# Kernel tuning notes

Measured on AMD Instinct MI355X. Metric: run time of the kernel, lower is better.

## Reference

```python
import jax, jax.numpy as jnp
import numpy as np

B_SZ, T_LEN, VOCAB, R = 32, 500, 8192, 4

def setup_inputs() -> dict:
    key = jax.random.key(0)
    k1, k2, k3 = jax.random.split(key, 3)
    x = jax.random.normal(k1, (B_SZ, T_LEN, VOCAB), dtype=jnp.float32)
    Y = jax.random.randint(k2, (B_SZ, T_LEN), 0, VOCAB, dtype=jnp.int64)
    B_buf = jax.random.normal(k3, (R + 1,), dtype=jnp.float32)
    return {"x": x, "Y": Y, "B_buf": B_buf}

def reference(x, Y, B_buf):
    # Supervised InfoNCE at batch_num == 0 (A_neg buffer reset to -inf, B <- B_).
    x = jnp.clip(x, -30.0, 30.0)
    Bsz, T, V = x.shape
    # cross[i, j] = sum_t x[j, t, Y[i, t]]  (score of sample j's logits under sample i's targets)
    g = jnp.take_along_axis(x[None, :, :, :], Y[:, None, :, None], axis=3)[..., 0]  # [B_i, B_j, T]
    cross = g.sum(axis=2)  # [B, B]
    numerator = jnp.diagonal(cross)  # [B], cross[i,i] == gather(x_i, Y_i).sum
    # logaddexp(numerator[i], logsumexp_{j!=i} cross[i,j]) == logsumexp_j cross[i,j]
    denominator = jax.scipy.special.logsumexp(cross, axis=1)  # [B]
    # A_neg[i] = -inf at batch_num 0, so only B_buf[0] contributes extra mass
    denominator_ = jnp.logaddexp(denominator, B_buf[0])
    loss_terms = numerator - denominator_  # [B]
    correct = jnp.exp(loss_terms).sum() * T
    loss = -loss_terms.sum()
    loss = loss / (Bsz * T)  # avg=True; l2_reg=0
    return loss, correct
```

## Files before the change

kernel.cpp:

```cpp
#include <hip/hip_runtime.h>
#include <math.h>

#define B_SZ  32
#define T_LEN 500
#define VOCAB 8192

__global__ __launch_bounds__(256)
void infonce_cross_kernel(const float* __restrict__ x,
                          const int*   __restrict__ Y,
                          float*       __restrict__ cross) {
    const int j = blockIdx.x;
    const int i = blockIdx.y;
    const float* __restrict__ xj = x + (size_t)j * T_LEN * VOCAB;
    const int*   __restrict__ Yi = Y + i * T_LEN;

    float acc = 0.0f;
    for (int t = threadIdx.x; t < T_LEN; t += 256) {
        const int y = Yi[t];
        float v = xj[(size_t)t * VOCAB + y];
        v = fminf(fmaxf(v, -30.0f), 30.0f);
        acc += v;
    }

    #pragma unroll
    for (int off = 32; off > 0; off >>= 1)
        acc += __shfl_down(acc, off, 64);

    __shared__ float ws[4];
    const int lane = threadIdx.x & 63;
    const int wid  = threadIdx.x >> 6;
    if (lane == 0) ws[wid] = acc;
    __syncthreads();
    if (threadIdx.x == 0) {
        cross[i * B_SZ + j] = ws[0] + ws[1] + ws[2] + ws[3];
    }
}

__global__ __launch_bounds__(64)
void infonce_finalize_kernel(const float* __restrict__ cross,
                             const float* __restrict__ B_buf,
                             float*       __restrict__ out) {
    __shared__ double lt[B_SZ];
    const int i = threadIdx.x;

    if (i < B_SZ) {
        double m = -INFINITY;
        #pragma unroll
        for (int jj = 0; jj < B_SZ; ++jj) {
            double c = (double)cross[i * B_SZ + jj];
            m = fmax(m, c);
        }
        double s = 0.0;
        #pragma unroll
        for (int jj = 0; jj < B_SZ; ++jj) {
            s += exp((double)cross[i * B_SZ + jj] - m);
        }
        const double lse = m + log(s);
        const double b0 = (double)B_buf[0];
        const double hi = fmax(lse, b0);
        const double lo = fmin(lse, b0);
        const double den = hi + log1p(exp(lo - hi));
        const double num = (double)cross[i * B_SZ + i];
        lt[i] = num - den;
    }
    __syncthreads();

    if (i == 0) {
        double sum_lt = 0.0, sum_exp = 0.0;
        #pragma unroll
        for (int k = 0; k < B_SZ; ++k) {
            sum_lt  += lt[k];
            sum_exp += exp(lt[k]);
        }
        out[0] = (float)(-sum_lt / ((double)B_SZ * (double)T_LEN));
        out[1] = (float)(sum_exp * (double)T_LEN);
    }
}

extern "C" void kernel_launch(void* const* d_in, const int* in_sizes, int n_in,
                              void* d_out, int out_size, void* d_ws, size_t ws_size,
                              hipStream_t stream) {
    const float* x     = (const float*)d_in[0];
    const int*   Y     = (const int*)  d_in[1];
    const float* B_buf = (const float*)d_in[2];
    float* out = (float*)d_out;
    float* cross = (float*)d_ws;

    dim3 grid(B_SZ, B_SZ);
    infonce_cross_kernel<<<grid, 256, 0, stream>>>(x, Y, cross);
    infonce_finalize_kernel<<<1, 64, 0, stream>>>(cross, B_buf, out);
}
```

Baseline: 21.02 us.

## Fuse cross and finalize kernels with last-block atomic counter

```diff
diff --git a/kernel.cpp b/kernel.cpp
--- a/kernel.cpp
+++ b/kernel.cpp
@@ -1,79 +1,87 @@
 #include <hip/hip_runtime.h>
 #include <math.h>
 
-#define B_SZ  32
-#define T_LEN 500
-#define VOCAB 8192
+#define B_SZ   32
+#define T_LEN  500
+#define VOCAB  8192
+#define NBLK   (B_SZ * B_SZ)
 
-__global__ __launch_bounds__(256)
-void infonce_cross_kernel(const float* __restrict__ x,
+__global__ __launch_bounds__(512)
+void infonce_fused_kernel(const float* __restrict__ x,
                           const int*   __restrict__ Y,
-                          float*       __restrict__ cross) {
-    const int j = blockIdx.x;
-    const int i = blockIdx.y;
-    const float* __restrict__ xj = x + (size_t)j * T_LEN * VOCAB;
-    const int*   __restrict__ Yi = Y + i * T_LEN;
+                          const float* __restrict__ B_buf,
+                          float*       __restrict__ out,
+                          float*       __restrict__ cross,
+                          unsigned*    __restrict__ counter) {
+    const int j   = blockIdx.x;
+    const int i   = blockIdx.y;
+    const int tid = threadIdx.x;
 
     float acc = 0.0f;
-    for (int t = threadIdx.x; t < T_LEN; t += 256) {
-        const int y = Yi[t];
-        float v = xj[(size_t)t * VOCAB + y];
-        v = fminf(fmaxf(v, -30.0f), 30.0f);
-        acc += v;
+    if (tid < T_LEN) {
+        const int y = Y[i * T_LEN + tid];
+        float v = x[(size_t)j * T_LEN * VOCAB + (size_t)tid * VOCAB + y];
+        acc = fminf(fmaxf(v, -30.0f), 30.0f);
     }
 
     #pragma unroll
     for (int off = 32; off > 0; off >>= 1)
         acc += __shfl_down(acc, off, 64);
 
-    __shared__ float ws[4];
-    const int lane = threadIdx.x & 63;
-    const int wid  = threadIdx.x >> 6;
-    if (lane == 0) ws[wid] = acc;
+    __shared__ float ws[8];
+    __shared__ int   isLast;
+    if ((tid & 63) == 0) ws[tid >> 6] = acc;
     __syncthreads();
-    if (threadIdx.x == 0) {
-        cross[i * B_SZ + j] = ws[0] + ws[1] + ws[2] + ws[3];
+
+    if (tid == 0) {
+        float s = 0.0f;
+        #pragma unroll
+        for (int w = 0; w < 8; ++w) s += ws[w];
+        __hip_atomic_store(&cross[i * B_SZ + j], s,
+                           __ATOMIC_RELEASE, __HIP_MEMORY_SCOPE_AGENT);
+        unsigned prev = __hip_atomic_fetch_add(counter, 1u,
+                           __ATOMIC_ACQ_REL, __HIP_MEMORY_SCOPE_AGENT);
+        isLast = (prev == NBLK - 1);
     }
-}
+    __syncthreads();
+    if (!isLast) return;
 
-__global__ __launch_bounds__(64)
-void infonce_finalize_kernel(const float* __restrict__ cross,
-                             const float* __restrict__ B_buf,
-                             float*       __restrict__ out) {
-    __shared__ double lt[B_SZ];
-    const int i = threadIdx.x;
-
-    if (i < B_SZ) {
-        double m = -INFINITY;
+    __shared__ float lt[B_SZ];
+    if (tid < B_SZ) {
+        float m = -INFINITY;
         #pragma unroll
         for (int jj = 0; jj < B_SZ; ++jj) {
-            double c = (double)cross[i * B_SZ + jj];
-            m = fmax(m, c);
+            float c = __hip_atomic_load(&cross[tid * B_SZ + jj],
+                          __ATOMIC_RELAXED, __HIP_MEMORY_SCOPE_AGENT);
+            m = fmaxf(m, c);
         }
-        double s = 0.0;
+        float s = 0.0f;
         #pragma unroll
         for (int jj = 0; jj < B_SZ; ++jj) {
-            s += exp((double)cross[i * B_SZ + jj] - m);
+            float c = __hip_atomic_load(&cross[tid * B_SZ + jj],
+                          __ATOMIC_RELAXED, __HIP_MEMORY_SCOPE_AGENT);
+            s += expf(c - m);
         }
-        const double lse = m + log(s);
-        const double b0 = (double)B_buf[0];
-        const double hi = fmax(lse, b0);
-        const double lo = fmin(lse, b0);
-        const double den = hi + log1p(exp(lo - hi));
-        const double num = (double)cross[i * B_SZ + i];
-        lt[i] = num - den;
+        const float lse = m + logf(s);
+        const float b0  = B_buf[0];
+        const float hi  = fmaxf(lse, b0);
+        const float lo  = fminf(lse, b0);
+        const float den = hi + log1pf(expf(lo - hi));
+        const float num = __hip_atomic_load(&cross[tid * B_SZ + tid],
+                              __ATOMIC_RELAXED, __HIP_MEMORY_SCOPE_AGENT);
+        lt[tid] = num - den;
     }
     __syncthreads();
 
-    if (i == 0) {
-        double sum_lt = 0.0, sum_exp = 0.0;
+    if (tid == 0) {
+        float sum_lt = 0.0f, sum_exp = 0.0f;
         #pragma unroll
         for (int k = 0; k < B_SZ; ++k) {
             sum_lt  += lt[k];
-            sum_exp += exp(lt[k]);
+            sum_exp += expf(lt[k]);
         }
-        out[0] = (float)(-sum_lt / ((double)B_SZ * (double)T_LEN));
-        out[1] = (float)(sum_exp * (double)T_LEN);
+        out[0] = -sum_lt / ((float)B_SZ * (float)T_LEN);
+        out[1] = sum_exp * (float)T_LEN;
     }
 }
 
@@ -83,10 +91,12 @@
     const float* x     = (const float*)d_in[0];
     const int*   Y     = (const int*)  d_in[1];
     const float* B_buf = (const float*)d_in[2];
-    float* out = (float*)d_out;
-    float* cross = (float*)d_ws;
+    float*    out     = (float*)d_out;
+    float*    cross   = (float*)d_ws;
+    unsigned* counter = (unsigned*)((char*)d_ws + 4096);
+
+    hipMemsetAsync(counter, 0, sizeof(unsigned), stream);
 
     dim3 grid(B_SZ, B_SZ);
-    infonce_cross_kernel<<<grid, 256, 0, stream>>>(x, Y, cross);
-    infonce_finalize_kernel<<<1, 64, 0, stream>>>(cross, B_buf, out);
+    infonce_fused_kernel<<<grid, 512, 0, stream>>>(x, Y, B_buf, out, cross, counter);
 }
```

New measurement: 62.56 us. +197.7%, slower.
